# Optimization experiments

Hardware: AMD Instinct MI355X
Metric: run time of the kernel (lower is better)

## Reference

```python
import jax, jax.numpy as jnp
import numpy as np

N_HEAD = 4
GROUPS = 32
EPS = 1e-5


def group_norm(x, scale, bias):
    B, C, H, W = x.shape
    xg = x.reshape(B, GROUPS, C // GROUPS, H, W)
    mu = xg.mean(axis=(2, 3, 4), keepdims=True)
    var = xg.var(axis=(2, 3, 4), keepdims=True)
    xg = (xg - mu) * jax.lax.rsqrt(var + EPS)
    x = xg.reshape(B, C, H, W)
    return x * scale[None, :, None, None] + bias[None, :, None, None]


def setup_inputs() -> dict:
    key = jax.random.key(0)
    k0, k1, k2 = jax.random.split(key, 3)
    B, C, H, W = 2, 64, 64, 64
    x = jax.random.normal(k0, (B, C, H, W), dtype=jnp.float32)
    gn_scale = jnp.ones((C,), dtype=jnp.float32)
    gn_bias = jnp.zeros((C,), dtype=jnp.float32)
    w_qkv = jax.random.normal(k1, (3 * C, C), dtype=jnp.float32) * 0.05  # 1x1 conv, no bias
    w_out = jax.random.normal(k2, (C, C), dtype=jnp.float32) * 0.05     # 1x1 conv
    b_out = jnp.zeros((C,), dtype=jnp.float32)
    return {"x": x, "gn_scale": gn_scale, "gn_bias": gn_bias,
            "w_qkv": w_qkv, "w_out": w_out, "b_out": b_out}


def reference(x, gn_scale, gn_bias, w_qkv, w_out, b_out):
    B, C, H, W = x.shape
    head_dim = C // N_HEAD
    norm = group_norm(x, gn_scale, gn_bias)
    # 1x1 conv == channel matmul
    qkv = jnp.einsum('oc,bchw->bohw', w_qkv, norm)
    qkv = qkv.reshape(B, N_HEAD, head_dim * 3, H, W)
    q, k, v = jnp.split(qkv, 3, axis=2)  # each [B, n, head_dim, H, W]
    # full spatial attention scores, scaled by sqrt(channel) as in source
    attn = jnp.einsum('bnchw,bncyx->bnhwyx', q, k) / jnp.sqrt(jnp.float32(C))
    attn = jax.nn.softmax(attn.reshape(B, N_HEAD, H, W, H * W), axis=-1)
    attn = attn.reshape(B, N_HEAD, H, W, H, W)
    out = jnp.einsum('bnhwyx,bncyx->bnchw', attn, v).reshape(B, C, H, W)
    out = jnp.einsum('oc,bchw->bohw', w_out, out) + b_out[None, :, None, None]
    return out + x
```

## Files before the change

kernel.cpp:

```cpp
#include <hip/hip_runtime.h>
#include <hip/hip_bf16.h>

typedef __attribute__((ext_vector_type(8))) short short8;
typedef __attribute__((ext_vector_type(4))) float f32x4;
typedef __attribute__((ext_vector_type(16))) float f32x16;
typedef __attribute__((ext_vector_type(4))) unsigned int uint4v;

#define DEV static __device__ __forceinline__

DEV unsigned short f2bf(float f){
  unsigned u = __float_as_uint(f);
  u += 0x7fffu + ((u >> 16) & 1u);
  return (unsigned short)(u >> 16);
}

DEV unsigned pack2bf(float a, float b){
  __hip_bfloat162 h = __float22bfloat162_rn(make_float2(a, b));
  unsigned u;
  __builtin_memcpy(&u, &h, 4);
  return u;
}

#define QSCALE 0.180336880111f
#define NSPLIT 4
#define NT 16

__global__ __launch_bounds__(256) void gn_partial_k(const float* __restrict__ x,
                                                    float* __restrict__ gp){
  int blk = blockIdx.x;
  float4 v = ((const float4*)(x + (size_t)blk*1024))[threadIdx.x];
  float s = v.x+v.y+v.z+v.w;
  float q = v.x*v.x+v.y*v.y+v.z*v.z+v.w*v.w;
  #pragma unroll
  for (int off = 1; off < 64; off <<= 1){
    s += __shfl_xor(s, off);
    q += __shfl_xor(q, off);
  }
  __shared__ float red[8];
  int w = threadIdx.x >> 6;
  if ((threadIdx.x & 63) == 0){ red[w*2] = s; red[w*2+1] = q; }
  __syncthreads();
  if (threadIdx.x == 0){
    gp[blk*2+0] = red[0]+red[2]+red[4]+red[6];
    gp[blk*2+1] = red[1]+red[3]+red[5]+red[7];
  }
}

__global__ __launch_bounds__(256) void qkv_k(const float* __restrict__ x,
    const float* __restrict__ gp, const float* __restrict__ gsc,
    const float* __restrict__ gbi, const float* __restrict__ wq,
    unsigned short* __restrict__ q, unsigned short* __restrict__ k,
    unsigned short* __restrict__ vt){
  int b  = blockIdx.x >> 7;
  int s0 = (blockIdx.x & 127) * 32;
  __shared__ float W[192][68];
  __shared__ float A[32][68];
  __shared__ float MS[32][2];
  int t = threadIdx.x;
  for (int i = t; i < 3072; i += 256){
    int o = i >> 4, c4 = (i & 15) * 4;
    *(float4*)&W[o][c4] = ((const float4*)wq)[i];
  }
  if (t < 32){
    float s = 0.f, ss = 0.f;
    #pragma unroll
    for (int i = 0; i < 8; ++i){
      const float* pp = gp + ((b*32 + t)*8 + i)*2;
      s += pp[0]; ss += pp[1];
    }
    float mean = s * (1.f/8192.f);
    MS[t][0] = mean;
    MS[t][1] = rsqrtf(ss * (1.f/8192.f) - mean*mean + 1e-5f);
  }
  if (t < 128){
    int n = t >> 5, si = t & 31;
    vt[((size_t)(b*4 + n)*32 + 16)*4096 + s0 + si] = (unsigned short)0x3F80;
  }
  __syncthreads();
  {
    int c  = t >> 2;
    int s8 = (t & 3) * 8;
    const float* px = x + ((size_t)b*64 + c)*4096 + s0 + s8;
    float4 v0 = *(const float4*)px;
    float4 v1 = *(const float4*)(px + 4);
    float sc = gsc[c] * MS[c>>1][1];
    float bi = gbi[c] - MS[c>>1][0] * sc;
    A[s8+0][c]=v0.x*sc+bi; A[s8+1][c]=v0.y*sc+bi; A[s8+2][c]=v0.z*sc+bi; A[s8+3][c]=v0.w*sc+bi;
    A[s8+4][c]=v1.x*sc+bi; A[s8+5][c]=v1.y*sc+bi; A[s8+6][c]=v1.z*sc+bi; A[s8+7][c]=v1.w*sc+bi;
  }
  __syncthreads();
  int sl = t >> 3, grp = t & 7;
  float acc[24];
  #pragma unroll
  for (int j = 0; j < 24; ++j) acc[j] = 0.f;
  for (int c4 = 0; c4 < 16; ++c4){
    float4 a = *(const float4*)&A[sl][c4*4];
    #pragma unroll
    for (int j = 0; j < 24; ++j){
      float4 wv = *(const float4*)&W[grp + j*8][c4*4];
      acc[j] = fmaf(a.x, wv.x, fmaf(a.y, wv.y, fmaf(a.z, wv.z, fmaf(a.w, wv.w, acc[j]))));
    }
  }
  int s = s0 + sl;
  int slp = (sl & 0x13) | (((sl >> 2) & 1) << 3) | (((sl >> 3) & 1) << 2);
  #pragma unroll
  for (int j = 0; j < 24; ++j){
    int o = grp + j*8;
    int n = o / 48, r = o % 48;
    float val = acc[j];
    if (r < 16){
      q[((((size_t)b*4 + n)*4096 + s))*16 + r] = f2bf(val * QSCALE);
    } else if (r < 32){
      k[((((size_t)b*4 + n)*4096 + s))*16 + r - 16] = f2bf(val);
    } else {
      vt[((size_t)(b*4 + n)*32 + (r - 32))*4096 + s0 + slp] = f2bf(val);
    }
  }
}

__global__ __launch_bounds__(256) void attn_k(const unsigned short* __restrict__ qb,
    const unsigned short* __restrict__ kb, const unsigned short* __restrict__ vt,
    float* __restrict__ part, float* __restrict__ lsums){
  int blk = blockIdx.x;
  int bn = blk & 7;
  int sp = (blk >> 3) & (NSPLIT - 1);
  int qt = blk >> 5;
  int t = threadIdx.x, w = t >> 6, l = t & 63;
  int lq = l & 31, hi = l >> 5;

  const unsigned short* Kp = kb + ((size_t)bn*4096 + sp*(NT*64))*16;
  int vrow = (lq < 16) ? lq : 16;
  const unsigned short* Vr = vt + ((size_t)bn*32 + vrow)*4096 + sp*(NT*64) + hi*8;
  int qrow = qt*128 + w*32;
  const unsigned short* Qp = qb + ((size_t)bn*4096 + qrow)*16;

  short8 qf = *(const short8*)(Qp + (size_t)lq*16 + hi*8);
  const unsigned short* kaddr = Kp + (size_t)lq*16 + hi*8;

  f32x16 O, zero;
  #pragma unroll
  for (int r = 0; r < 16; ++r){ O[r] = 0.f; zero[r] = 0.f; }

  short8 kf0 = *(const short8*)(kaddr);
  short8 kf1 = *(const short8*)(kaddr + 512);
  short8 vf0 = *(const short8*)(Vr);
  short8 vf1 = *(const short8*)(Vr + 16);
  short8 vf2 = *(const short8*)(Vr + 32);
  short8 vf3 = *(const short8*)(Vr + 48);

  for (int kt = 0; kt < NT; ++kt){
    bool pf = (kt + 1) < NT;
    short8 kn0 = {}, kn1 = {}, vn0 = {}, vn1 = {}, vn2 = {}, vn3 = {};
    if (pf){
      const unsigned short* ka = kaddr + (size_t)(kt+1)*1024;
      kn0 = *(const short8*)(ka);
      kn1 = *(const short8*)(ka + 512);
      const unsigned short* va = Vr + (size_t)(kt+1)*64;
      vn0 = *(const short8*)(va);
      vn1 = *(const short8*)(va + 16);
      vn2 = *(const short8*)(va + 32);
      vn3 = *(const short8*)(va + 48);
    }

    f32x16 sA = __builtin_amdgcn_mfma_f32_32x32x16_bf16(kf0, qf, zero, 0, 0, 0);
    f32x16 sB = __builtin_amdgcn_mfma_f32_32x32x16_bf16(kf1, qf, zero, 0, 0, 0);

    #pragma unroll
    for (int r = 0; r < 16; ++r) sA[r] = __builtin_amdgcn_exp2f(sA[r]);
    #pragma unroll
    for (int r = 0; r < 16; ++r) sB[r] = __builtin_amdgcn_exp2f(sB[r]);

    auto pvstep = [&](const f32x16& pc, int h8, short8 vf){
      uint4v pw;
      pw[0] = pack2bf(pc[h8+0], pc[h8+1]);
      pw[1] = pack2bf(pc[h8+2], pc[h8+3]);
      pw[2] = pack2bf(pc[h8+4], pc[h8+5]);
      pw[3] = pack2bf(pc[h8+6], pc[h8+7]);
      short8 pa = __builtin_bit_cast(short8, pw);
      O = __builtin_amdgcn_mfma_f32_32x32x16_bf16(pa, vf, O, 0, 0, 0);
    };
    pvstep(sA, 0, vf0);
    pvstep(sA, 8, vf1);
    pvstep(sB, 0, vf2);
    pvstep(sB, 8, vf3);

    kf0 = kn0; kf1 = kn1;
    vf0 = vn0; vf1 = vn1; vf2 = vn2; vf3 = vn3;
  }

  float* Op = part + (((size_t)sp*8 + bn)*4096 + qrow)*16;
  size_t lbase = ((size_t)sp*8 + bn)*4096 + qrow;
  #pragma unroll
  for (int r = 0; r < 16; ++r){
    int qr = (r&3) + 8*(r>>2) + 4*hi;
    if (lq < 16) __builtin_nontemporal_store(O[r], &Op[(size_t)qr*16 + lq]);
  }
  if (lq == 16){
    #pragma unroll
    for (int r = 0; r < 16; ++r){
      int qr = (r&3) + 8*(r>>2) + 4*hi;
      __builtin_nontemporal_store(O[r], &lsums[lbase + qr]);
    }
  }
}

__global__ __launch_bounds__(256) void oproj_k(const float* __restrict__ part,
    const float* __restrict__ lsums, const float* __restrict__ wo,
    const float* __restrict__ bo, const float* __restrict__ x,
    float* __restrict__ out){
  int b  = blockIdx.x >> 8;
  int s0 = (blockIdx.x & 255) * 16;
  __shared__ float W[64][68];
  __shared__ float A[16][68];
  int t = threadIdx.x;
  for (int i = t; i < 1024; i += 256){
    int o = i >> 4, c4 = (i & 15) * 4;
    *(float4*)&W[o][c4] = ((const float4*)wo)[i];
  }
  {
    int sl = t & 15;
    int u  = t >> 4;
    int n = u >> 2, d4 = (u & 3) * 4;
    size_t row = ((size_t)b*4 + n)*4096 + s0 + sl;
    float L = 0.f;
    #pragma unroll
    for (int sp = 0; sp < NSPLIT; ++sp)
      L += __builtin_nontemporal_load(&lsums[(size_t)sp*32768 + row]);
    f32x4 acc = {0.f,0.f,0.f,0.f};
    #pragma unroll
    for (int sp = 0; sp < NSPLIT; ++sp){
      f32x4 u0 = __builtin_nontemporal_load(
          (const f32x4*)(part + ((size_t)sp*32768 + row)*16 + d4));
      acc += u0;
    }
    float inv = 1.f / L;
    A[sl][n*16+d4+0] = acc[0]*inv; A[sl][n*16+d4+1] = acc[1]*inv;
    A[sl][n*16+d4+2] = acc[2]*inv; A[sl][n*16+d4+3] = acc[3]*inv;
  }
  __syncthreads();
  int sl = t & 15, grp = t >> 4;
  float acc[4] = {0.f,0.f,0.f,0.f};
  for (int c4 = 0; c4 < 16; ++c4){
    float4 a = *(const float4*)&A[sl][c4*4];
    #pragma unroll
    for (int j = 0; j < 4; ++j){
      float4 wv = *(const float4*)&W[grp + j*16][c4*4];
      acc[j] = fmaf(a.x, wv.x, fmaf(a.y, wv.y, fmaf(a.z, wv.z, fmaf(a.w, wv.w, acc[j]))));
    }
  }
  int s = s0 + sl;
  #pragma unroll
  for (int j = 0; j < 4; ++j){
    int o = grp + j*16;
    size_t idx = ((size_t)b*64 + o)*4096 + s;
    out[idx] = acc[j] + bo[o] + x[idx];
  }
}

extern "C" void kernel_launch(void* const* d_in, const int* in_sizes, int n_in,
                              void* d_out, int out_size, void* d_ws, size_t ws_size,
                              hipStream_t stream){
  const float* x   = (const float*)d_in[0];
  const float* gsc = (const float*)d_in[1];
  const float* gbi = (const float*)d_in[2];
  const float* wq  = (const float*)d_in[3];
  const float* wo  = (const float*)d_in[4];
  const float* bo  = (const float*)d_in[5];
  float* out = (float*)d_out;

  char* ws = (char*)d_ws;
  float* gp          = (float*)ws;
  unsigned short* q  = (unsigned short*)(ws + 8192);
  unsigned short* k  = (unsigned short*)(ws + 8192 + 1048576);
  unsigned short* vt = (unsigned short*)(ws + 8192 + 2097152);
  float* part        = (float*)(ws + 8192 + 4194304);
  float* lsums       = (float*)(ws + 8192 + 4194304 + 8388608);

  gn_partial_k<<<512,  256, 0, stream>>>(x, gp);
  qkv_k       <<<256,  256, 0, stream>>>(x, gp, gsc, gbi, wq, q, k, vt);
  attn_k      <<<1024, 256, 0, stream>>>(q, k, vt, part, lsums);
  oproj_k     <<<512,  256, 0, stream>>>(part, lsums, wo, bo, x, out);
}
```

Before: 55.68 us.

## Reuse K/V tiles across two query tiles and split keys eightfold

The attention kernel now has each wave process 64 query rows as two 32-row MFMA tiles that share the same K and V fragments. This halves K/V loads per query. The key range is split into 8 parts of 8 tiles each, so the grid stays at 1024 blocks while each block does less sequential work. The ones-column used to accumulate the softmax denominator is now built in registers instead of being written into vt by qkv_k, which shrinks vt to 16 rows; qkv_k also switches to 16-position blocks with twice as many blocks. In exchange, the V prefetch is dropped (V is loaded in the same iteration it is used), the partial-sum buffers double in size, and the combine step must reduce more partials.

```diff
diff --git a/kernel.cpp b/kernel.cpp
--- a/kernel.cpp
+++ b/kernel.cpp
@@ -22,8 +22,8 @@
 }
 
 #define QSCALE 0.180336880111f
-#define NSPLIT 4
-#define NT 16
+#define NSPLIT 8
+#define NT 8
 
 __global__ __launch_bounds__(256) void gn_partial_k(const float* __restrict__ x,
                                                     float* __restrict__ gp){
@@ -51,10 +51,10 @@
     const float* __restrict__ gbi, const float* __restrict__ wq,
     unsigned short* __restrict__ q, unsigned short* __restrict__ k,
     unsigned short* __restrict__ vt){
-  int b  = blockIdx.x >> 7;
-  int s0 = (blockIdx.x & 127) * 32;
+  int b  = blockIdx.x >> 8;
+  int s0 = (blockIdx.x & 255) * 16;
   __shared__ float W[192][68];
-  __shared__ float A[32][68];
+  __shared__ float A[16][68];
   __shared__ float MS[32][2];
   int t = threadIdx.x;
   for (int i = t; i < 3072; i += 256){
@@ -72,105 +72,98 @@
     MS[t][0] = mean;
     MS[t][1] = rsqrtf(ss * (1.f/8192.f) - mean*mean + 1e-5f);
   }
-  if (t < 128){
-    int n = t >> 5, si = t & 31;
-    vt[((size_t)(b*4 + n)*32 + 16)*4096 + s0 + si] = (unsigned short)0x3F80;
-  }
   __syncthreads();
   {
     int c  = t >> 2;
-    int s8 = (t & 3) * 8;
-    const float* px = x + ((size_t)b*64 + c)*4096 + s0 + s8;
+    int s4 = (t & 3) * 4;
+    const float* px = x + ((size_t)b*64 + c)*4096 + s0 + s4;
     float4 v0 = *(const float4*)px;
-    float4 v1 = *(const float4*)(px + 4);
     float sc = gsc[c] * MS[c>>1][1];
     float bi = gbi[c] - MS[c>>1][0] * sc;
-    A[s8+0][c]=v0.x*sc+bi; A[s8+1][c]=v0.y*sc+bi; A[s8+2][c]=v0.z*sc+bi; A[s8+3][c]=v0.w*sc+bi;
-    A[s8+4][c]=v1.x*sc+bi; A[s8+5][c]=v1.y*sc+bi; A[s8+6][c]=v1.z*sc+bi; A[s8+7][c]=v1.w*sc+bi;
-  }
-  __syncthreads();
-  int sl = t >> 3, grp = t & 7;
-  float acc[24];
-  #pragma unroll
-  for (int j = 0; j < 24; ++j) acc[j] = 0.f;
+    A[s4+0][c]=v0.x*sc+bi; A[s4+1][c]=v0.y*sc+bi;
+    A[s4+2][c]=v0.z*sc+bi; A[s4+3][c]=v0.w*sc+bi;
+  }
+  __syncthreads();
+  int sl = t >> 4, grp = t & 15;
+  float acc[12];
+  #pragma unroll
+  for (int j = 0; j < 12; ++j) acc[j] = 0.f;
   for (int c4 = 0; c4 < 16; ++c4){
     float4 a = *(const float4*)&A[sl][c4*4];
     #pragma unroll
-    for (int j = 0; j < 24; ++j){
-      float4 wv = *(const float4*)&W[grp + j*8][c4*4];
+    for (int j = 0; j < 12; ++j){
+      float4 wv = *(const float4*)&W[grp + j*16][c4*4];
       acc[j] = fmaf(a.x, wv.x, fmaf(a.y, wv.y, fmaf(a.z, wv.z, fmaf(a.w, wv.w, acc[j]))));
     }
   }
   int s = s0 + sl;
-  int slp = (sl & 0x13) | (((sl >> 2) & 1) << 3) | (((sl >> 3) & 1) << 2);
-  #pragma unroll
-  for (int j = 0; j < 24; ++j){
-    int o = grp + j*8;
+  int slp = (sl & 0x3) | (((sl >> 2) & 1) << 3) | (((sl >> 3) & 1) << 2);
+  #pragma unroll
+  for (int j = 0; j < 12; ++j){
+    int o = grp + j*16;
     int n = o / 48, r = o % 48;
     float val = acc[j];
     if (r < 16){
-      q[((((size_t)b*4 + n)*4096 + s))*16 + r] = f2bf(val * QSCALE);
+      q[(((size_t)b*4 + n)*4096 + s)*16 + r] = f2bf(val * QSCALE);
     } else if (r < 32){
-      k[((((size_t)b*4 + n)*4096 + s))*16 + r - 16] = f2bf(val);
+      k[(((size_t)b*4 + n)*4096 + s)*16 + r - 16] = f2bf(val);
     } else {
-      vt[((size_t)(b*4 + n)*32 + (r - 32))*4096 + s0 + slp] = f2bf(val);
-    }
-  }
-}
-
-__global__ __launch_bounds__(256) void attn_k(const unsigned short* __restrict__ qb,
+      vt[((size_t)(b*4 + n)*16 + (r - 32))*4096 + s0 + slp] = f2bf(val);
+    }
+  }
+}
+
+__global__ __launch_bounds__(256, 4) void attn_k(const unsigned short* __restrict__ qb,
     const unsigned short* __restrict__ kb, const unsigned short* __restrict__ vt,
     float* __restrict__ part, float* __restrict__ lsums){
   int blk = blockIdx.x;
   int bn = blk & 7;
   int sp = (blk >> 3) & (NSPLIT - 1);
-  int qt = blk >> 5;
+  int qt = blk >> 6;
   int t = threadIdx.x, w = t >> 6, l = t & 63;
   int lq = l & 31, hi = l >> 5;
 
-  const unsigned short* Kp = kb + ((size_t)bn*4096 + sp*(NT*64))*16;
-  int vrow = (lq < 16) ? lq : 16;
-  const unsigned short* Vr = vt + ((size_t)bn*32 + vrow)*4096 + sp*(NT*64) + hi*8;
-  int qrow = qt*128 + w*32;
+  const unsigned short* kaddr = kb + ((size_t)bn*4096 + sp*(NT*64) + lq)*16 + hi*8;
+  const unsigned short* vaddr = vt + ((size_t)bn*16 + (lq & 15))*4096 + sp*(NT*64) + hi*8;
+  bool vld = (lq < 16);
+  int qrow = qt*256 + w*64;
   const unsigned short* Qp = qb + ((size_t)bn*4096 + qrow)*16;
 
-  short8 qf = *(const short8*)(Qp + (size_t)lq*16 + hi*8);
-  const unsigned short* kaddr = Kp + (size_t)lq*16 + hi*8;
-
-  f32x16 O, zero;
-  #pragma unroll
-  for (int r = 0; r < 16; ++r){ O[r] = 0.f; zero[r] = 0.f; }
+  short8 qf0 = *(const short8*)(Qp + (size_t)lq*16 + hi*8);
+  short8 qf1 = *(const short8*)(Qp + (size_t)(32 + lq)*16 + hi*8);
+
+  f32x16 O0, O1, zero;
+  #pragma unroll
+  for (int r = 0; r < 16; ++r){ O0[r] = 0.f; O1[r] = 0.f; zero[r] = 0.f; }
+
+  short8 vsel;
+  {
+    unsigned short c = (lq == 16) ? (unsigned short)0x3F80 : (unsigned short)0;
+    #pragma unroll
+    for (int r = 0; r < 8; ++r) vsel[r] = (short)c;
+  }
 
   short8 kf0 = *(const short8*)(kaddr);
   short8 kf1 = *(const short8*)(kaddr + 512);
-  short8 vf0 = *(const short8*)(Vr);
-  short8 vf1 = *(const short8*)(Vr + 16);
-  short8 vf2 = *(const short8*)(Vr + 32);
-  short8 vf3 = *(const short8*)(Vr + 48);
-
+
+  #pragma unroll 1
   for (int kt = 0; kt < NT; ++kt){
-    bool pf = (kt + 1) < NT;
-    short8 kn0 = {}, kn1 = {}, vn0 = {}, vn1 = {}, vn2 = {}, vn3 = {};
-    if (pf){
+    short8 v0 = vsel, v1 = vsel, v2 = vsel, v3 = vsel;
+    if (vld){
+      const unsigned short* va = vaddr + (size_t)kt*64;
+      v0 = *(const short8*)(va);
+      v1 = *(const short8*)(va + 16);
+      v2 = *(const short8*)(va + 32);
+      v3 = *(const short8*)(va + 48);
+    }
+    short8 kn0 = {}, kn1 = {};
+    if (kt + 1 < NT){
       const unsigned short* ka = kaddr + (size_t)(kt+1)*1024;
       kn0 = *(const short8*)(ka);
       kn1 = *(const short8*)(ka + 512);
-      const unsigned short* va = Vr + (size_t)(kt+1)*64;
-      vn0 = *(const short8*)(va);
-      vn1 = *(const short8*)(va + 16);
-      vn2 = *(const short8*)(va + 32);
-      vn3 = *(const short8*)(va + 48);
-    }
-
-    f32x16 sA = __builtin_amdgcn_mfma_f32_32x32x16_bf16(kf0, qf, zero, 0, 0, 0);
-    f32x16 sB = __builtin_amdgcn_mfma_f32_32x32x16_bf16(kf1, qf, zero, 0, 0, 0);
-
-    #pragma unroll
-    for (int r = 0; r < 16; ++r) sA[r] = __builtin_amdgcn_exp2f(sA[r]);
-    #pragma unroll
-    for (int r = 0; r < 16; ++r) sB[r] = __builtin_amdgcn_exp2f(sB[r]);
-
-    auto pvstep = [&](const f32x16& pc, int h8, short8 vf){
+    }
+
+    auto pvstep = [&](f32x16& O, const f32x16& pc, int h8, short8 vf){
       uint4v pw;
       pw[0] = pack2bf(pc[h8+0], pc[h8+1]);
       pw[1] = pack2bf(pc[h8+2], pc[h8+3]);
@@ -179,13 +172,29 @@
       short8 pa = __builtin_bit_cast(short8, pw);
       O = __builtin_amdgcn_mfma_f32_32x32x16_bf16(pa, vf, O, 0, 0, 0);
     };
-    pvstep(sA, 0, vf0);
-    pvstep(sA, 8, vf1);
-    pvstep(sB, 0, vf2);
-    pvstep(sB, 8, vf3);
+
+    {
+      f32x16 sA = __builtin_amdgcn_mfma_f32_32x32x16_bf16(kf0, qf0, zero, 0, 0, 0);
+      f32x16 sB = __builtin_amdgcn_mfma_f32_32x32x16_bf16(kf1, qf0, zero, 0, 0, 0);
+      #pragma unroll
+      for (int r = 0; r < 16; ++r) sA[r] = __builtin_amdgcn_exp2f(sA[r]);
+      #pragma unroll
+      for (int r = 0; r < 16; ++r) sB[r] = __builtin_amdgcn_exp2f(sB[r]);
+      pvstep(O0, sA, 0, v0); pvstep(O0, sA, 8, v1);
+      pvstep(O0, sB, 0, v2); pvstep(O0, sB, 8, v3);
+    }
+    {
+      f32x16 sA = __builtin_amdgcn_mfma_f32_32x32x16_bf16(kf0, qf1, zero, 0, 0, 0);
+      f32x16 sB = __builtin_amdgcn_mfma_f32_32x32x16_bf16(kf1, qf1, zero, 0, 0, 0);
+      #pragma unroll
+      for (int r = 0; r < 16; ++r) sA[r] = __builtin_amdgcn_exp2f(sA[r]);
+      #pragma unroll
+      for (int r = 0; r < 16; ++r) sB[r] = __builtin_amdgcn_exp2f(sB[r]);
+      pvstep(O1, sA, 0, v0); pvstep(O1, sA, 8, v1);
+      pvstep(O1, sB, 0, v2); pvstep(O1, sB, 8, v3);
+    }
 
     kf0 = kn0; kf1 = kn1;
-    vf0 = vn0; vf1 = vn1; vf2 = vn2; vf3 = vn3;
   }
 
   float* Op = part + (((size_t)sp*8 + bn)*4096 + qrow)*16;
@@ -193,13 +202,17 @@
   #pragma unroll
   for (int r = 0; r < 16; ++r){
     int qr = (r&3) + 8*(r>>2) + 4*hi;
-    if (lq < 16) __builtin_nontemporal_store(O[r], &Op[(size_t)qr*16 + lq]);
+    if (lq < 16){
+      __builtin_nontemporal_store(O0[r], &Op[(size_t)qr*16 + lq]);
+      __builtin_nontemporal_store(O1[r], &Op[(size_t)(32 + qr)*16 + lq]);
+    }
   }
   if (lq == 16){
     #pragma unroll
     for (int r = 0; r < 16; ++r){
       int qr = (r&3) + 8*(r>>2) + 4*hi;
-      __builtin_nontemporal_store(O[r], &lsums[lbase + qr]);
+      __builtin_nontemporal_store(O0[r], &lsums[lbase + qr]);
+      __builtin_nontemporal_store(O1[r], &lsums[lbase + 32 + qr]);
     }
   }
 }
@@ -273,11 +286,11 @@
   unsigned short* q  = (unsigned short*)(ws + 8192);
   unsigned short* k  = (unsigned short*)(ws + 8192 + 1048576);
   unsigned short* vt = (unsigned short*)(ws + 8192 + 2097152);
-  float* part        = (float*)(ws + 8192 + 4194304);
-  float* lsums       = (float*)(ws + 8192 + 4194304 + 8388608);
+  float* part        = (float*)(ws + 8192 + 3145728);
+  float* lsums       = (float*)(ws + 8192 + 3145728 + 16777216);
 
   gn_partial_k<<<512,  256, 0, stream>>>(x, gp);
-  qkv_k       <<<256,  256, 0, stream>>>(x, gp, gsc, gbi, wq, q, k, vt);
+  qkv_k       <<<512,  256, 0, stream>>>(x, gp, gsc, gbi, wq, q, k, vt);
   attn_k      <<<1024, 256, 0, stream>>>(q, k, vt, part, lsums);
   oproj_k     <<<512,  256, 0, stream>>>(part, lsums, wo, bo, x, out);
 }
```

Result: slower. 58.18 us (+4.5%).
